# Kernel tuning notes

Hardware: AMD Instinct MI355X
Metric: run time of the kernel (lower is better)

The kernel has to match this reference:

```python
import jax, jax.numpy as jnp
import numpy as np

N_USERS = 100000
EMBED = 128
N_NODES = 10000
N_EDGES = 320000


def setup_inputs() -> dict:
    key = jax.random.key(0)
    ks = jax.random.split(key, 10)
    nodes = jax.random.randint(ks[0], (N_NODES,), 0, N_USERS, dtype=jnp.int64) if jax.config.jax_enable_x64 else jax.random.randint(ks[0], (N_NODES,), 0, N_USERS)
    neigh_idx = jax.random.randint(ks[1], (N_EDGES,), 0, N_USERS)
    seg_ids = jnp.sort(jax.random.randint(ks[2], (N_EDGES,), 0, N_NODES))
    u2e = jax.random.normal(ks[3], (N_USERS, EMBED), jnp.float32) * 0.02
    s1 = 1.0 / np.sqrt(2 * EMBED)
    s2 = 1.0 / np.sqrt(EMBED)
    att1_w = jax.random.uniform(ks[4], (EMBED, 2 * EMBED), jnp.float32, -s1, s1)
    att1_b = jnp.zeros((EMBED,), jnp.float32)
    att2_w = jax.random.uniform(ks[5], (EMBED, EMBED), jnp.float32, -s2, s2)
    att2_b = jnp.zeros((EMBED,), jnp.float32)
    att3_w = jax.random.uniform(ks[6], (1, EMBED), jnp.float32, -s2, s2)
    att3_b = jnp.zeros((1,), jnp.float32)
    return dict(nodes=nodes, neigh_idx=neigh_idx, seg_ids=seg_ids, u2e=u2e,
                att1_w=att1_w, att1_b=att1_b, att2_w=att2_w, att2_b=att2_b,
                att3_w=att3_w, att3_b=att3_b)


def reference(nodes, neigh_idx, seg_ids, u2e, att1_w, att1_b, att2_w, att2_b, att3_w, att3_b):
    # CSR-style ragged neighborhood attention (GraphRec Social_Aggregator).
    e_u = u2e[neigh_idx]                               # [E, D] neighbor embeddings
    u_rep = u2e[nodes][seg_ids]                        # [E, D] center-node embedding per edge
    x = jnp.concatenate([e_u, u_rep], axis=1)          # [E, 2D]
    h = jax.nn.relu(x @ att1_w.T + att1_b)             # [E, D]
    h = jax.nn.relu(h @ att2_w.T + att2_b)             # [E, D]
    s = (h @ att3_w.T + att3_b)[:, 0]                  # [E] unnormalized scores
    # segment softmax over each node's neighbors (dim=0 softmax per segment)
    m = jax.ops.segment_max(s, seg_ids, num_segments=N_NODES)
    e = jnp.exp(s - m[seg_ids])
    denom = jax.ops.segment_sum(e, seg_ids, num_segments=N_NODES)
    w = e / denom[seg_ids]                             # [E] attention weights
    agg = jax.ops.segment_sum(w[:, None] * e_u, seg_ids, num_segments=N_NODES)  # [N, D]
    # zero-degree fallback: embed_matrix[i] = u2e[nodes[i]]
    counts = jax.ops.segment_sum(jnp.ones_like(s), seg_ids, num_segments=N_NODES)
    return jnp.where(counts[:, None] > 0, agg, u2e[nodes])
```

## Files before the change

kernel.cpp:

```cpp
#include <hip/hip_runtime.h>

#define EMBED 128
#define NEDGES 320000
#define NNODES 10000
#define NUSERS 100000
#define PBLK3 1563
#define QBLK3 157

typedef __attribute__((ext_vector_type(4))) float f32x4;
typedef __attribute__((ext_vector_type(8))) short bf16x8;

__device__ __forceinline__ short f2bf(float f) {
  union { float f; unsigned u; } v; v.f = f;
  unsigned r = v.u + 0x7fffu + ((v.u >> 16) & 1u);
  return (short)(r >> 16);
}
__device__ __forceinline__ float bf2f(short s) {
  union { unsigned u; float f; } v;
  v.u = ((unsigned)(unsigned short)s) << 16;
  return v.f;
}

__global__ __launch_bounds__(256) void prep_kernel(
    const int* __restrict__ seg_ids, const float* __restrict__ w1,
    const float* __restrict__ w2, int* __restrict__ off,
    short* __restrict__ w1a, short* __restrict__ w1b, short* __restrict__ w2bf) {
  int tid = blockIdx.x * 256 + threadIdx.x;
  if (tid < NEDGES) {
    int cur = seg_ids[tid];
    int prev = (tid == 0) ? -1 : seg_ids[tid - 1];
    for (int n = prev + 1; n <= cur; ++n) off[n] = tid;
    if (tid == NEDGES - 1)
      for (int n = cur + 1; n <= NNODES; ++n) off[n] = NEDGES;
  }
  if (tid < 128 * 256) {
    int n = tid >> 8, k = tid & 255;
    int kk = k & 127;
    int ks = kk >> 5, g = (kk >> 2) & 3, h = (kk >> 4) & 1, j = kk & 3;
    short* dst = (k < 128) ? w1a : w1b;
    dst[(((ks * 4 + g) * 128 + n) << 3) + (h << 2) + j] = f2bf(w1[tid]);
  }
  if (tid < 128 * 128) {
    int n = tid >> 7, kk = tid & 127;
    int ks = kk >> 5, g = (kk >> 2) & 3, h = (kk >> 4) & 1, j = kk & 3;
    w2bf[(((ks * 4 + g) * 128 + n) << 3) + (h << 2) + j] = f2bf(w2[tid]);
  }
}

__global__ __launch_bounds__(256) void row_gemm3_kernel(
    const float* __restrict__ u2e, const int* __restrict__ nodes,
    const short* __restrict__ w1a, const short* __restrict__ w1b,
    const float* __restrict__ b1,
    short* __restrict__ P_sw, short* __restrict__ Q_sw) {
  __shared__ short lds[16384];

  const int tid = threadIdx.x;
  const int lane = tid & 63, wv = tid >> 6;
  const int g = lane >> 4, lm = lane & 15;

  const bool isQ = blockIdx.x >= PBLK3;
  const int blk = isQ ? (int)blockIdx.x - PBLK3 : (int)blockIdx.x;
  const int nrows = isQ ? NNODES : NUSERS;
  const short* wbf = isQ ? w1b : w1a;
  short* out = isQ ? Q_sw : P_sw;

#pragma unroll
  for (int i = 0; i < 8; ++i) {
    int o = (i * 256 + tid) << 3;
    *(bf16x8*)&lds[o] = *(const bf16x8*)&wbf[o];
  }
  __syncthreads();

  const int rb = blk * 64 + wv * 16;

  {
  }
  int row = rb + lm;
  int rc = row < nrows ? row : nrows - 1;
  const float* src = u2e + (size_t)(isQ ? nodes[rc] : rc) * EMBED;
  bf16x8 af[4];
#pragma unroll
  for (int ks = 0; ks < 4; ++ks) {
    const float* p = src + 32 * ks + 4 * g;
    f32x4 lo = *(const f32x4*)p;
    f32x4 hi = *(const f32x4*)(p + 16);
    bf16x8 a;
    a[0] = f2bf(lo.x); a[1] = f2bf(lo.y); a[2] = f2bf(lo.z); a[3] = f2bf(lo.w);
    a[4] = f2bf(hi.x); a[5] = f2bf(hi.y); a[6] = f2bf(hi.z); a[7] = f2bf(hi.w);
    af[ks] = a;
  }

  f32x4 acc[8];
#pragma unroll
  for (int nt = 0; nt < 8; ++nt) acc[nt] = (f32x4){0.f, 0.f, 0.f, 0.f};

#pragma unroll
  for (int ks = 0; ks < 4; ++ks) {
#pragma unroll
    for (int nt = 0; nt < 8; ++nt) {
      bf16x8 b = *(const bf16x8*)&lds[((((ks * 4 + g) * 128) + nt * 16 + lm) << 3)];
      acc[nt] = __builtin_amdgcn_mfma_f32_16x16x32_bf16(af[ks], b, acc[nt], 0, 0, 0);
    }
  }
  __syncthreads();

  short* st = &lds[wv * 2176];
#pragma unroll
  for (int nt = 0; nt < 8; ++nt) {
    float bs = isQ ? b1[nt * 16 + lm] : 0.f;
    int fragoff = (((nt >> 1) * 4 + (lm >> 2)) << 3) + ((nt & 1) << 2) + (lm & 3);
#pragma unroll
    for (int r = 0; r < 4; ++r)
      st[(4 * g + r) * 136 + fragoff] = f2bf(acc[nt][r] + bs);
  }
  asm volatile("s_waitcnt lgkmcnt(0)" ::: "memory");

  const int srow = lane >> 2, q = lane & 3;
  const int u = rb + srow;
  if (u < nrows) {
    short* orow = out + (size_t)u * 128 + q * 32;
    const short* sr = st + srow * 136 + q * 32;
#pragma unroll
    for (int i = 0; i < 4; ++i)
      *(bf16x8*)(orow + i * 8) = *(const bf16x8*)(sr + i * 8);
  }
}

__global__ __launch_bounds__(256) void scores2_kernel(
    const int* __restrict__ neigh_idx, const int* __restrict__ seg_ids,
    const short* __restrict__ P_sw, const short* __restrict__ Q_sw,
    const short* __restrict__ w2bf, const float* __restrict__ b2,
    const float* __restrict__ w3v, const float* __restrict__ b3,
    float* __restrict__ s_out) {
  const int lane = threadIdx.x & 63, wv = threadIdx.x >> 6;
  const int g = lane >> 4, lm = lane & 15;
  const int eb = (blockIdx.x * 4 + wv) * 32;

  bf16x8 h1[2][4];
#pragma unroll
  for (int mt = 0; mt < 2; ++mt) {
    int e = eb + mt * 16 + lm;
    const short* pb = P_sw + (size_t)neigh_idx[e] * 128;
    const short* qb = Q_sw + (size_t)seg_ids[e] * 128;
#pragma unroll
    for (int ks = 0; ks < 4; ++ks) {
      bf16x8 pa = *(const bf16x8*)(pb + ((ks * 4 + g) << 3));
      bf16x8 qa = *(const bf16x8*)(qb + ((ks * 4 + g) << 3));
      bf16x8 hh;
#pragma unroll
      for (int i = 0; i < 8; ++i)
        hh[i] = f2bf(fmaxf(bf2f(pa[i]) + bf2f(qa[i]), 0.f));
      h1[mt][ks] = hh;
    }
  }

  f32x4 acc2[2][8];
#pragma unroll
  for (int mt = 0; mt < 2; ++mt)
#pragma unroll
    for (int nt = 0; nt < 8; ++nt) acc2[mt][nt] = (f32x4){0.f, 0.f, 0.f, 0.f};

#pragma unroll
  for (int ks = 0; ks < 4; ++ks) {
#pragma unroll
    for (int nt = 0; nt < 8; ++nt) {
      bf16x8 b = *(const bf16x8*)(w2bf + ((((ks * 4 + g) * 128) + nt * 16 + lm) << 3));
      acc2[0][nt] = __builtin_amdgcn_mfma_f32_16x16x32_bf16(h1[0][ks], b, acc2[0][nt], 0, 0, 0);
      acc2[1][nt] = __builtin_amdgcn_mfma_f32_16x16x32_bf16(h1[1][ks], b, acc2[1][nt], 0, 0, 0);
    }
  }

  float part[2][4] = {{0.f, 0.f, 0.f, 0.f}, {0.f, 0.f, 0.f, 0.f}};
#pragma unroll
  for (int nt = 0; nt < 8; ++nt) {
    int n = nt * 16 + lm;
    float bias = b2[n];
    float w3n = w3v[n];
#pragma unroll
    for (int mt = 0; mt < 2; ++mt)
#pragma unroll
      for (int r = 0; r < 4; ++r) {
        float h2 = fmaxf(acc2[mt][nt][r] + bias, 0.f);
        part[mt][r] += h2 * w3n;
      }
  }
#pragma unroll
  for (int off = 1; off < 16; off <<= 1)
#pragma unroll
    for (int mt = 0; mt < 2; ++mt)
#pragma unroll
      for (int r = 0; r < 4; ++r)
        part[mt][r] += __shfl_xor(part[mt][r], off, 64);
  if (lm == 0) {
    float b3s = b3[0];
#pragma unroll
    for (int mt = 0; mt < 2; ++mt)
#pragma unroll
      for (int r = 0; r < 4; ++r)
        s_out[eb + mt * 16 + 4 * g + r] = part[mt][r] + b3s;
  }
}

__global__ __launch_bounds__(256) void agg2_kernel(
    const int* __restrict__ nodes, const int* __restrict__ neigh_idx,
    const float* __restrict__ u2e, const float* __restrict__ s,
    const int* __restrict__ off, float* __restrict__ out) {
  const int lane = threadIdx.x & 63, wv = threadIdx.x >> 6;
  const int node = blockIdx.x * 4 + wv;
  const int lo = off[node], hi = off[node + 1];
  float* orow = out + (size_t)node * EMBED;

  if (lo >= hi) {
    const float* src = u2e + (size_t)nodes[node] * EMBED;
    orow[lane] = src[lane];
    orow[lane + 64] = src[lane + 64];
    return;
  }

  float mx = -3.402823466e38f;
  for (int e = lo + lane; e < hi; e += 64) mx = fmaxf(mx, s[e]);
#pragma unroll
  for (int o = 32; o >= 1; o >>= 1) mx = fmaxf(mx, __shfl_xor(mx, o, 64));

  float sum = 0.f;
  for (int e = lo + lane; e < hi; e += 64) sum += expf(s[e] - mx);
#pragma unroll
  for (int o = 32; o >= 1; o >>= 1) sum += __shfl_xor(sum, o, 64);
  const float inv = 1.0f / sum;

  const int eg = lane >> 4, ld = lane & 15;
  f32x4 a0 = (f32x4){0.f, 0.f, 0.f, 0.f};
  f32x4 a1 = (f32x4){0.f, 0.f, 0.f, 0.f};
  for (int e = lo + eg; e < hi; e += 4) {
    float w = expf(s[e] - mx) * inv;
    const float* row = u2e + (size_t)neigh_idx[e] * EMBED + ld * 8;
    f32x4 r0 = *(const f32x4*)row;
    f32x4 r1 = *(const f32x4*)(row + 4);
    a0 += w * r0;
    a1 += w * r1;
  }
#pragma unroll
  for (int o = 16; o <= 32; o <<= 1) {
#pragma unroll
    for (int c = 0; c < 4; ++c) {
      a0[c] += __shfl_xor(a0[c], o, 64);
      a1[c] += __shfl_xor(a1[c], o, 64);
    }
  }
  if (eg == 0) {
    *(f32x4*)(orow + ld * 8) = a0;
    *(f32x4*)(orow + ld * 8 + 4) = a1;
  }
}

extern "C" void kernel_launch(void* const* d_in, const int* in_sizes, int n_in,
                              void* d_out, int out_size, void* d_ws, size_t ws_size,
                              hipStream_t stream) {
  const int* nodes  = (const int*)d_in[0];
  const int* neigh  = (const int*)d_in[1];
  const int* segs   = (const int*)d_in[2];
  const float* u2e  = (const float*)d_in[3];
  const float* w1   = (const float*)d_in[4];
  const float* b1   = (const float*)d_in[5];
  const float* w2   = (const float*)d_in[6];
  const float* b2   = (const float*)d_in[7];
  const float* w3   = (const float*)d_in[8];
  const float* b3   = (const float*)d_in[9];
  float* out = (float*)d_out;

  char* ws = (char*)d_ws;
  short* w1a  = (short*)(ws);
  short* w1b  = (short*)(ws + 32768);
  short* w2bf = (short*)(ws + 65536);
  float* s    = (float*)(ws + 98304);
  int*   off  = (int*)(ws + 1378304);
  short* P_sw = (short*)(ws + 1418752);
  short* Q_sw = (short*)(ws + 27018752);

  hipLaunchKernelGGL(prep_kernel, dim3(1250), dim3(256), 0, stream,
                     segs, w1, w2, off, w1a, w1b, w2bf);
  hipLaunchKernelGGL(row_gemm3_kernel, dim3(PBLK3 + QBLK3), dim3(256), 0, stream,
                     u2e, nodes, w1a, w1b, b1, P_sw, Q_sw);
  hipLaunchKernelGGL(scores2_kernel, dim3(2500), dim3(256), 0, stream,
                     neigh, segs, P_sw, Q_sw, w2bf, b2, w3, b3, s);
  hipLaunchKernelGGL(agg2_kernel, dim3(2500), dim3(256), 0, stream,
                     nodes, neigh, u2e, s, off, out);
}
```

Baseline: 177.0 us.

## Fuse score MLP and segment-softmax aggregation into one per-node online-softmax kernel

Merges the edge-score kernel and the aggregation kernel into a single per-node kernel. It computes scores in 32-edge chunks with MFMA against W2 staged in LDS and runs an online softmax with a running max and denominator. The row GEMM now also writes a bf16 copy of each u2e row, interleaved next to its P row, so the aggregation gathers half-size bf16 neighbor rows from the same cache lines instead of fp32 u2e. This removes the score round trip to global memory and one kernel launch, and halves gather bytes in aggregation. In exchange the neighbor embeddings lose precision (bf16 instead of fp32), h1 uses truncating rounding, and low-degree nodes leave wave lanes underused.

```diff
diff --git a/kernel.cpp b/kernel.cpp
--- a/kernel.cpp
+++ b/kernel.cpp
@@ -9,11 +9,16 @@
 
 typedef __attribute__((ext_vector_type(4))) float f32x4;
 typedef __attribute__((ext_vector_type(8))) short bf16x8;
+typedef __attribute__((ext_vector_type(4))) short bf16x4;
 
 __device__ __forceinline__ short f2bf(float f) {
   union { float f; unsigned u; } v; v.f = f;
   unsigned r = v.u + 0x7fffu + ((v.u >> 16) & 1u);
   return (short)(r >> 16);
+}
+__device__ __forceinline__ short f2bf_trunc(float f) {
+  union { float f; unsigned u; } v; v.f = f;
+  return (short)(v.u >> 16);
 }
 __device__ __forceinline__ float bf2f(short s) {
   union { unsigned u; float f; } v;
@@ -47,11 +52,11 @@
   }
 }
 
-__global__ __launch_bounds__(256) void row_gemm3_kernel(
+__global__ __launch_bounds__(256) void row_gemm4_kernel(
     const float* __restrict__ u2e, const int* __restrict__ nodes,
     const short* __restrict__ w1a, const short* __restrict__ w1b,
     const float* __restrict__ b1,
-    short* __restrict__ P_sw, short* __restrict__ Q_sw) {
+    short* __restrict__ PU, short* __restrict__ Q_sw) {
   __shared__ short lds[16384];
 
   const int tid = threadIdx.x;
@@ -62,7 +67,6 @@
   const int blk = isQ ? (int)blockIdx.x - PBLK3 : (int)blockIdx.x;
   const int nrows = isQ ? NNODES : NUSERS;
   const short* wbf = isQ ? w1b : w1a;
-  short* out = isQ ? Q_sw : P_sw;
 
 #pragma unroll
   for (int i = 0; i < 8; ++i) {
@@ -72,9 +76,6 @@
   __syncthreads();
 
   const int rb = blk * 64 + wv * 16;
-
-  {
-  }
   int row = rb + lm;
   int rc = row < nrows ? row : nrows - 1;
   const float* src = u2e + (size_t)(isQ ? nodes[rc] : rc) * EMBED;
@@ -88,6 +89,11 @@
     a[0] = f2bf(lo.x); a[1] = f2bf(lo.y); a[2] = f2bf(lo.z); a[3] = f2bf(lo.w);
     a[4] = f2bf(hi.x); a[5] = f2bf(hi.y); a[6] = f2bf(hi.z); a[7] = f2bf(hi.w);
     af[ks] = a;
+    if (!isQ) {
+      short* dst = PU + (size_t)rc * 256 + 128 + 32 * ks + 4 * g;
+      *(bf16x4*)dst = (bf16x4){a[0], a[1], a[2], a[3]};
+      *(bf16x4*)(dst + 16) = (bf16x4){a[4], a[5], a[6], a[7]};
+    }
   }
 
   f32x4 acc[8];
@@ -118,7 +124,7 @@
   const int srow = lane >> 2, q = lane & 3;
   const int u = rb + srow;
   if (u < nrows) {
-    short* orow = out + (size_t)u * 128 + q * 32;
+    short* orow = (isQ ? Q_sw + (size_t)u * 128 : PU + (size_t)u * 256) + q * 32;
     const short* sr = st + srow * 136 + q * 32;
 #pragma unroll
     for (int i = 0; i < 4; ++i)
@@ -126,86 +132,26 @@
   }
 }
 
-__global__ __launch_bounds__(256) void scores2_kernel(
-    const int* __restrict__ neigh_idx, const int* __restrict__ seg_ids,
-    const short* __restrict__ P_sw, const short* __restrict__ Q_sw,
-    const short* __restrict__ w2bf, const float* __restrict__ b2,
-    const float* __restrict__ w3v, const float* __restrict__ b3,
-    float* __restrict__ s_out) {
-  const int lane = threadIdx.x & 63, wv = threadIdx.x >> 6;
+__global__ __launch_bounds__(256) void fused_sagg_kernel(
+    const int* __restrict__ nodes, const int* __restrict__ neigh_idx,
+    const int* __restrict__ off, const short* __restrict__ PU,
+    const short* __restrict__ Q_sw, const short* __restrict__ w2bf,
+    const float* __restrict__ b2, const float* __restrict__ w3v,
+    const float* __restrict__ u2e, float* __restrict__ out) {
+  __shared__ short w2l[16384];
+  __shared__ float sbuf[4][32];
+
+  const int tid = threadIdx.x;
+  const int lane = tid & 63, wv = tid >> 6;
   const int g = lane >> 4, lm = lane & 15;
-  const int eb = (blockIdx.x * 4 + wv) * 32;
-
-  bf16x8 h1[2][4];
-#pragma unroll
-  for (int mt = 0; mt < 2; ++mt) {
-    int e = eb + mt * 16 + lm;
-    const short* pb = P_sw + (size_t)neigh_idx[e] * 128;
-    const short* qb = Q_sw + (size_t)seg_ids[e] * 128;
-#pragma unroll
-    for (int ks = 0; ks < 4; ++ks) {
-      bf16x8 pa = *(const bf16x8*)(pb + ((ks * 4 + g) << 3));
-      bf16x8 qa = *(const bf16x8*)(qb + ((ks * 4 + g) << 3));
-      bf16x8 hh;
-#pragma unroll
-      for (int i = 0; i < 8; ++i)
-        hh[i] = f2bf(fmaxf(bf2f(pa[i]) + bf2f(qa[i]), 0.f));
-      h1[mt][ks] = hh;
-    }
-  }
-
-  f32x4 acc2[2][8];
-#pragma unroll
-  for (int mt = 0; mt < 2; ++mt)
-#pragma unroll
-    for (int nt = 0; nt < 8; ++nt) acc2[mt][nt] = (f32x4){0.f, 0.f, 0.f, 0.f};
-
-#pragma unroll
-  for (int ks = 0; ks < 4; ++ks) {
-#pragma unroll
-    for (int nt = 0; nt < 8; ++nt) {
-      bf16x8 b = *(const bf16x8*)(w2bf + ((((ks * 4 + g) * 128) + nt * 16 + lm) << 3));
-      acc2[0][nt] = __builtin_amdgcn_mfma_f32_16x16x32_bf16(h1[0][ks], b, acc2[0][nt], 0, 0, 0);
-      acc2[1][nt] = __builtin_amdgcn_mfma_f32_16x16x32_bf16(h1[1][ks], b, acc2[1][nt], 0, 0, 0);
-    }
-  }
-
-  float part[2][4] = {{0.f, 0.f, 0.f, 0.f}, {0.f, 0.f, 0.f, 0.f}};
-#pragma unroll
-  for (int nt = 0; nt < 8; ++nt) {
-    int n = nt * 16 + lm;
-    float bias = b2[n];
-    float w3n = w3v[n];
-#pragma unroll
-    for (int mt = 0; mt < 2; ++mt)
-#pragma unroll
-      for (int r = 0; r < 4; ++r) {
-        float h2 = fmaxf(acc2[mt][nt][r] + bias, 0.f);
-        part[mt][r] += h2 * w3n;
-      }
-  }
-#pragma unroll
-  for (int off = 1; off < 16; off <<= 1)
-#pragma unroll
-    for (int mt = 0; mt < 2; ++mt)
-#pragma unroll
-      for (int r = 0; r < 4; ++r)
-        part[mt][r] += __shfl_xor(part[mt][r], off, 64);
-  if (lm == 0) {
-    float b3s = b3[0];
-#pragma unroll
-    for (int mt = 0; mt < 2; ++mt)
-#pragma unroll
-      for (int r = 0; r < 4; ++r)
-        s_out[eb + mt * 16 + 4 * g + r] = part[mt][r] + b3s;
-  }
-}
-
-__global__ __launch_bounds__(256) void agg2_kernel(
-    const int* __restrict__ nodes, const int* __restrict__ neigh_idx,
-    const float* __restrict__ u2e, const float* __restrict__ s,
-    const int* __restrict__ off, float* __restrict__ out) {
-  const int lane = threadIdx.x & 63, wv = threadIdx.x >> 6;
+
+#pragma unroll
+  for (int i = 0; i < 8; ++i) {
+    int o = (i * 256 + tid) << 3;
+    *(bf16x8*)&w2l[o] = *(const bf16x8*)&w2bf[o];
+  }
+  __syncthreads();
+
   const int node = blockIdx.x * 4 + wv;
   const int lo = off[node], hi = off[node + 1];
   float* orow = out + (size_t)node * EMBED;
@@ -217,39 +163,119 @@
     return;
   }
 
-  float mx = -3.402823466e38f;
-  for (int e = lo + lane; e < hi; e += 64) mx = fmaxf(mx, s[e]);
-#pragma unroll
-  for (int o = 32; o >= 1; o >>= 1) mx = fmaxf(mx, __shfl_xor(mx, o, 64));
-
-  float sum = 0.f;
-  for (int e = lo + lane; e < hi; e += 64) sum += expf(s[e] - mx);
-#pragma unroll
-  for (int o = 32; o >= 1; o >>= 1) sum += __shfl_xor(sum, o, 64);
-  const float inv = 1.0f / sum;
-
-  const int eg = lane >> 4, ld = lane & 15;
+  const short* qb = Q_sw + (size_t)node * 128;
+  bf16x8 qf[4];
+#pragma unroll
+  for (int ks = 0; ks < 4; ++ks)
+    qf[ks] = *(const bf16x8*)(qb + ((ks * 4 + g) << 3));
+
+  float m_run = -3.402823466e38f, d_run = 0.f;
   f32x4 a0 = (f32x4){0.f, 0.f, 0.f, 0.f};
   f32x4 a1 = (f32x4){0.f, 0.f, 0.f, 0.f};
-  for (int e = lo + eg; e < hi; e += 4) {
-    float w = expf(s[e] - mx) * inv;
-    const float* row = u2e + (size_t)neigh_idx[e] * EMBED + ld * 8;
-    f32x4 r0 = *(const f32x4*)row;
-    f32x4 r1 = *(const f32x4*)(row + 4);
-    a0 += w * r0;
-    a1 += w * r1;
-  }
-#pragma unroll
-  for (int o = 16; o <= 32; o <<= 1) {
+
+  for (int base = lo; base < hi; base += 32) {
+    bf16x8 h1[2][4];
+#pragma unroll
+    for (int mt = 0; mt < 2; ++mt) {
+      int e = base + mt * 16 + lm;
+      int ec = e < hi ? e : hi - 1;
+      const short* pb = PU + (size_t)neigh_idx[ec] * 256;
+#pragma unroll
+      for (int ks = 0; ks < 4; ++ks) {
+        bf16x8 pa = *(const bf16x8*)(pb + ((ks * 4 + g) << 3));
+        bf16x8 hh;
+#pragma unroll
+        for (int i = 0; i < 8; ++i)
+          hh[i] = f2bf_trunc(fmaxf(bf2f(pa[i]) + bf2f(qf[ks][i]), 0.f));
+        h1[mt][ks] = hh;
+      }
+    }
+
+    f32x4 acc2[2][8];
+#pragma unroll
+    for (int mt = 0; mt < 2; ++mt)
+#pragma unroll
+      for (int nt = 0; nt < 8; ++nt) acc2[mt][nt] = (f32x4){0.f, 0.f, 0.f, 0.f};
+#pragma unroll
+    for (int ks = 0; ks < 4; ++ks) {
+#pragma unroll
+      for (int nt = 0; nt < 8; ++nt) {
+        bf16x8 b = *(const bf16x8*)&w2l[((((ks * 4 + g) * 128) + nt * 16 + lm) << 3)];
+        acc2[0][nt] = __builtin_amdgcn_mfma_f32_16x16x32_bf16(h1[0][ks], b, acc2[0][nt], 0, 0, 0);
+        acc2[1][nt] = __builtin_amdgcn_mfma_f32_16x16x32_bf16(h1[1][ks], b, acc2[1][nt], 0, 0, 0);
+      }
+    }
+
+    float part[2][4] = {{0.f, 0.f, 0.f, 0.f}, {0.f, 0.f, 0.f, 0.f}};
+#pragma unroll
+    for (int nt = 0; nt < 8; ++nt) {
+      int n = nt * 16 + lm;
+      float bias = b2[n];
+      float w3n = w3v[n];
+#pragma unroll
+      for (int mt = 0; mt < 2; ++mt)
+#pragma unroll
+        for (int r = 0; r < 4; ++r)
+          part[mt][r] += fmaxf(acc2[mt][nt][r] + bias, 0.f) * w3n;
+    }
+#pragma unroll
+    for (int o2 = 1; o2 < 16; o2 <<= 1)
+#pragma unroll
+      for (int mt = 0; mt < 2; ++mt)
+#pragma unroll
+        for (int r = 0; r < 4; ++r)
+          part[mt][r] += __shfl_xor(part[mt][r], o2, 64);
+    if (lm == 0) {
+      *(f32x4*)&sbuf[wv][4 * g] =
+          (f32x4){part[0][0], part[0][1], part[0][2], part[0][3]};
+      *(f32x4*)&sbuf[wv][16 + 4 * g] =
+          (f32x4){part[1][0], part[1][1], part[1][2], part[1][3]};
+    }
+    asm volatile("s_waitcnt lgkmcnt(0)" ::: "memory");
+
+    int slot = lane & 31;
+    float sv = sbuf[wv][slot];
+    bool valid = (lane < 32) && (base + slot < hi);
+    float mx = valid ? sv : -3.402823466e38f;
+#pragma unroll
+    for (int o2 = 1; o2 <= 32; o2 <<= 1) mx = fmaxf(mx, __shfl_xor(mx, o2, 64));
+    float m_new = fmaxf(m_run, mx);
+    float ex = valid ? __expf(sv - m_new) : 0.f;
+#pragma unroll
+    for (int o2 = 1; o2 <= 32; o2 <<= 1) ex += __shfl_xor(ex, o2, 64);
+    float scale = __expf(m_run - m_new);
+    d_run = d_run * scale + ex;
+    a0 *= scale;
+    a1 *= scale;
+    m_run = m_new;
+
+    for (int sl = g; sl < 32; sl += 4) {
+      int e = base + sl;
+      if (e >= hi) break;
+      float w = __expf(sbuf[wv][sl] - m_new);
+      bf16x8 r = *(const bf16x8*)(PU + (size_t)neigh_idx[e] * 256 + 128 + lm * 8);
+#pragma unroll
+      for (int c = 0; c < 4; ++c) {
+        a0[c] += w * bf2f(r[c]);
+        a1[c] += w * bf2f(r[c + 4]);
+      }
+    }
+  }
+
+  float inv = 1.0f / d_run;
+  a0 *= inv;
+  a1 *= inv;
+#pragma unroll
+  for (int o2 = 16; o2 <= 32; o2 <<= 1) {
 #pragma unroll
     for (int c = 0; c < 4; ++c) {
-      a0[c] += __shfl_xor(a0[c], o, 64);
-      a1[c] += __shfl_xor(a1[c], o, 64);
-    }
-  }
-  if (eg == 0) {
-    *(f32x4*)(orow + ld * 8) = a0;
-    *(f32x4*)(orow + ld * 8 + 4) = a1;
+      a0[c] += __shfl_xor(a0[c], o2, 64);
+      a1[c] += __shfl_xor(a1[c], o2, 64);
+    }
+  }
+  if (g == 0) {
+    *(f32x4*)(orow + lm * 8) = a0;
+    *(f32x4*)(orow + lm * 8 + 4) = a1;
   }
 }
 
@@ -265,24 +291,20 @@
   const float* w2   = (const float*)d_in[6];
   const float* b2   = (const float*)d_in[7];
   const float* w3   = (const float*)d_in[8];
-  const float* b3   = (const float*)d_in[9];
   float* out = (float*)d_out;
 
   char* ws = (char*)d_ws;
   short* w1a  = (short*)(ws);
   short* w1b  = (short*)(ws + 32768);
   short* w2bf = (short*)(ws + 65536);
-  float* s    = (float*)(ws + 98304);
-  int*   off  = (int*)(ws + 1378304);
-  short* P_sw = (short*)(ws + 1418752);
-  short* Q_sw = (short*)(ws + 27018752);
+  int*   off  = (int*)(ws + 98304);
+  short* PU   = (short*)(ws + 139264);
+  short* Q_sw = (short*)(ws + 139264 + 51200000);
 
   hipLaunchKernelGGL(prep_kernel, dim3(1250), dim3(256), 0, stream,
                      segs, w1, w2, off, w1a, w1b, w2bf);
-  hipLaunchKernelGGL(row_gemm3_kernel, dim3(PBLK3 + QBLK3), dim3(256), 0, stream,
-                     u2e, nodes, w1a, w1b, b1, P_sw, Q_sw);
-  hipLaunchKernelGGL(scores2_kernel, dim3(2500), dim3(256), 0, stream,
-                     neigh, segs, P_sw, Q_sw, w2bf, b2, w3, b3, s);
-  hipLaunchKernelGGL(agg2_kernel, dim3(2500), dim3(256), 0, stream,
-                     nodes, neigh, u2e, s, off, out);
-}
+  hipLaunchKernelGGL(row_gemm4_kernel, dim3(PBLK3 + QBLK3), dim3(256), 0, stream,
+                     u2e, nodes, w1a, w1b, b1, PU, Q_sw);
+  hipLaunchKernelGGL(fused_sagg_kernel, dim3(2500), dim3(256), 0, stream,
+                     nodes, neigh, off, PU, Q_sw, w2bf, b2, w3, u2e, out);
+}
```

Measured after the change: 202.0 us. +14.2%, slower.
